# Kernel tuning notes

Hardware: AMD Instinct MI355X
Metric: run time of the kernel (lower is better)

## Reference

```python
import jax, jax.numpy as jnp
import numpy as np

D_MODEL, D_FF, H, DK, DV = 1024, 4096, 16, 64, 64
B, S = 16, 512
EPS = 1e-6

def layer_norm(x, g, b):
    mu = jnp.mean(x, axis=-1, keepdims=True)
    var = jnp.var(x, axis=-1, keepdims=True)
    return (x - mu) / jnp.sqrt(var + EPS) * g + b

def setup_inputs() -> dict:
    key = jax.random.key(0)
    ks = jax.random.split(key, 16)
    def lin(k, fan_in, fan_out):
        lim = 1.0 / np.sqrt(fan_in)
        kw, kb = jax.random.split(k)
        W = jax.random.uniform(kw, (fan_in, fan_out), jnp.float32, -lim, lim)
        b = jax.random.uniform(kb, (fan_out,), jnp.float32, -lim, lim)
        return W, b
    Wq, bq = lin(ks[0], D_MODEL, DK * H)
    Wk, bk = lin(ks[1], D_MODEL, DK * H)
    Wv, bv = lin(ks[2], D_MODEL, DV * H)
    Wo, bo = lin(ks[3], DV * H, D_MODEL)
    w1, b1 = lin(ks[4], D_MODEL, D_FF)   # conv1d k=1 == pointwise linear
    w2, b2 = lin(ks[5], D_FF, D_MODEL)
    return {
        "enc_inputs": jax.random.normal(ks[6], (B, S, D_MODEL), jnp.float32),
        "Wq": Wq, "bq": bq, "Wk": Wk, "bk": bk, "Wv": Wv, "bv": bv,
        "Wo": Wo, "bo": bo,
        "ln1_g": jnp.ones((D_MODEL,), jnp.float32), "ln1_b": jnp.zeros((D_MODEL,), jnp.float32),
        "w1": w1, "b1": b1, "w2": w2, "b2": b2,
        "ln2_g": jnp.ones((D_MODEL,), jnp.float32), "ln2_b": jnp.zeros((D_MODEL,), jnp.float32),
        "mask": jax.random.randint(ks[7], (B, S), 0, 2, jnp.int32),
        "max_neighbors": S,
    }

def reference(enc_inputs, Wq, bq, Wk, bk, Wv, bv, Wo, bo, ln1_g, ln1_b,
              w1, b1, w2, b2, ln2_g, ln2_b, mask, max_neighbors):
    x = enc_inputs  # [B, S, D]
    residual = x
    # projections -> [B, H, S, d]
    q = (x @ Wq + bq).reshape(B, S, H, DK).transpose(0, 2, 1, 3)
    k = (x @ Wk + bk).reshape(B, S, H, DK).transpose(0, 2, 1, 3)
    v = (x @ Wv + bv).reshape(B, S, H, DV).transpose(0, 2, 1, 3)
    scores = jnp.einsum('bhqd,bhkd->bhqk', q, k) / np.sqrt(DK)
    pad = (mask == 0)[:, None, None, :]  # [B,1,1,S] broadcasts over heads & query
    scores = jnp.where(pad, jnp.float32(-1e9), scores)
    attn = jax.nn.softmax(scores, axis=-1)
    ctx = jnp.einsum('bhqk,bhkd->bhqd', attn, v)
    ctx = ctx.transpose(0, 2, 1, 3).reshape(B, S, H * DV)
    ctx = ctx @ Wo + bo
    ctx = layer_norm(ctx + residual, ln1_g, ln1_b)
    # position-wise FFN (conv1d kernel=1 == linear)
    ff = jax.nn.relu(ctx @ w1 + b1) @ w2 + b2
    out = layer_norm(ff + ctx, ln2_g, ln2_b)
    return out, attn
```

## Files before the change

### kernel.cpp

```cpp
#include <hip/hip_runtime.h>
#include <hip/hip_bf16.h>

typedef unsigned short u16;
typedef __bf16 bf16x8 __attribute__((ext_vector_type(8)));
typedef float f32x4 __attribute__((ext_vector_type(4)));

static __device__ __forceinline__ float b2f(u16 x) {
    unsigned int u = ((unsigned int)x) << 16;
    float f; __builtin_memcpy(&f, &u, 4); return f;
}
static __device__ __forceinline__ float b2f_u32(unsigned int u) {
    float f; __builtin_memcpy(&f, &u, 4); return f;
}
static __device__ __forceinline__ u16 f2b(float f) {
    unsigned int u; __builtin_memcpy(&u, &f, 4);
    unsigned int lsb = (u >> 16) & 1u;
    u += 0x7fffu + lsb;
    return (u16)(u >> 16);
}

static __device__ __forceinline__ void gload16(const u16* g, u16* l) {
    __builtin_amdgcn_global_load_lds(
        (const __attribute__((address_space(1))) unsigned int*)g,
        (__attribute__((address_space(3))) unsigned int*)l, 16, 0, 0);
}

__global__ __launch_bounds__(256) void transpose_f2b(const float* __restrict__ src,
                                                     u16* __restrict__ dst,
                                                     int R, int C) {
    __shared__ u16 tile[32][33];
    int c0 = blockIdx.x * 32, r0 = blockIdx.y * 32;
    int tx = threadIdx.x & 31, ty = threadIdx.x >> 5;
    for (int i = ty; i < 32; i += 8) {
        int r = r0 + i, c = c0 + tx;
        tile[i][tx] = (r < R && c < C) ? f2b(src[(long)r * C + c]) : (u16)0;
    }
    __syncthreads();
    for (int i = ty; i < 32; i += 8) {
        int c = c0 + i, r = r0 + tx;
        if (c < C && r < R) dst[(long)c * R + r] = tile[tx][i];
    }
}

__global__ __launch_bounds__(256) void concat3(const float* a, const float* b, const float* c,
                                               float* out) {
    int i = blockIdx.x * 256 + threadIdx.x;
    if (i < 1024) out[i] = a[i];
    else if (i < 2048) out[i] = b[i - 1024];
    else if (i < 3072) out[i] = c[i - 2048];
}

__global__ __launch_bounds__(256) void conv_f2b(const float* __restrict__ src,
                                                u16* __restrict__ dst, long n) {
    long i = ((long)blockIdx.x * 256 + threadIdx.x) * 4;
    if (i >= n) return;
    float4 f = *(const float4*)(src + i);
    ushort4 o;
    o.x = f2b(f.x); o.y = f2b(f.y); o.z = f2b(f.z); o.w = f2b(f.w);
    *(ushort4*)(dst + i) = o;
}

__global__ __launch_bounds__(512, 1) void gemm_bt256(
    const u16* __restrict__ A, const u16* __restrict__ B,
    const float* __restrict__ bias, u16* __restrict__ C,
    int M, int N, int K, int lda, int ldb, int ldc, int relu, int nbx) {
    __shared__ __align__(16) u16 lds[2][4][8192];

    int nwg = gridDim.x;
    int id = blockIdx.x;
    int swz = (id & 7) * (nwg >> 3) + (id >> 3);
    int bx = swz % nbx, by = swz / nbx;
    long m0 = (long)by * 256, n0 = (long)bx * 256;

    int tid = threadIdx.x, lane = tid & 63, wave = tid >> 6;
    int lrow = lane & 15, quad = lane >> 4;
    int wm2 = wave >> 2;
    int wn2 = wave & 3;

    int laneRd = (lrow * 64 + quad * 16) ^ (((lrow >> 3) & 1) << 5);
    int Sl = (lane * 16) ^ (((lane >> 5) & 1) << 5);
    int wr = (Sl >> 6) & 15;
    int wb = Sl & 63;

    f32x4 acc[8][4];
#pragma unroll
    for (int i = 0; i < 8; i++)
#pragma unroll
        for (int j = 0; j < 4; j++) acc[i][j] = (f32x4){0.f, 0.f, 0.f, 0.f};
    bf16x8 af[4][2], bfr[2][2];

#define STAGE_HT(nb, ht, kt) do {                                              \
    const char* _gb = ((ht) < 2)                                               \
        ? (const char*)(A + (m0 + (ht) * 128) * lda)                           \
        : (const char*)(B + (n0 + ((ht) - 2) * 128) * ldb);                    \
    long _ld = (long)(((ht) < 2) ? lda : ldb) * 2;                             \
    _Pragma("unroll")                                                          \
    for (int j = 0; j < 2; j++) {                                              \
        int sub = j * 8 + wave;                                                \
        int srow = (sub >> 1) * 16 + wr;                                       \
        int scolb = (sub & 1) * 64 + wb;                                       \
        gload16((const u16*)(_gb + (long)srow * _ld + (long)(kt) * 128 + scolb),\
                &lds[nb][ht][sub << 9]);                                       \
    }                                                                          \
} while (0)

#define DSLOAD_A(qm) do {                                                      \
    const char* _p = _ab + ((qm) << 14);                                       \
    _Pragma("unroll") for (int mi = 0; mi < 4; mi++)                           \
    _Pragma("unroll") for (int kk = 0; kk < 2; kk++)                           \
        af[mi][kk] = *(const bf16x8*)(_p + ((mi * 4 + kk) << 10));             \
} while (0)

#define DSLOAD_B(qn) do {                                                      \
    const char* _p = _bb + ((qn) << 14);                                       \
    _Pragma("unroll") for (int ni = 0; ni < 2; ni++)                           \
    _Pragma("unroll") for (int kk = 0; kk < 2; kk++)                           \
        bfr[ni][kk] = *(const bf16x8*)(_p + ((ni * 8 + kk) << 10));            \
} while (0)

#define DOMFMA(qm, qn) do {                                                    \
    __builtin_amdgcn_s_setprio(1);                                             \
    _Pragma("unroll") for (int mi = 0; mi < 4; mi++)                           \
    _Pragma("unroll") for (int ni = 0; ni < 2; ni++)                           \
    _Pragma("unroll") for (int kk = 0; kk < 2; kk++)                           \
        acc[(qm) * 4 + mi][(qn) * 2 + ni] =                                    \
            __builtin_amdgcn_mfma_f32_16x16x32_bf16(                           \
                af[mi][kk], bfr[ni][kk], acc[(qm) * 4 + mi][(qn) * 2 + ni],    \
                0, 0, 0);                                                      \
    __builtin_amdgcn_s_setprio(0);                                             \
} while (0)

#define MIDBAR()  do { __builtin_amdgcn_s_barrier(); __builtin_amdgcn_sched_barrier(0); } while (0)
#define ENDBAR()  do { __builtin_amdgcn_sched_barrier(0); __builtin_amdgcn_s_barrier(); } while (0)

    int NT = K >> 6;
    STAGE_HT(0, 0, 0);
    STAGE_HT(0, 2, 0);
    STAGE_HT(0, 1, 0);
    STAGE_HT(0, 3, 0);

    for (int t = 0; t < NT - 1; t++) {
        int cur = t & 1, nxt = cur ^ 1;
        const char* _ab = (const char*)&lds[cur][0][0] + (wm2 << 11) + laneRd;
        const char* _bb = (const char*)&lds[cur][2][0] + (wn2 << 11) + laneRd;
        STAGE_HT(nxt, 0, t + 1);
        asm volatile("s_waitcnt vmcnt(6)" ::: "memory");
        MIDBAR();
        DSLOAD_A(0); DSLOAD_B(0); DOMFMA(0, 0);
        ENDBAR();
        STAGE_HT(nxt, 2, t + 1);
        asm volatile("s_waitcnt vmcnt(6)" ::: "memory");
        MIDBAR();
        DSLOAD_A(1); DOMFMA(1, 0);
        ENDBAR();
        STAGE_HT(nxt, 1, t + 1);
        asm volatile("s_waitcnt vmcnt(6)" ::: "memory");
        MIDBAR();
        DSLOAD_B(1); DOMFMA(1, 1);
        ENDBAR();
        STAGE_HT(nxt, 3, t + 1);
        MIDBAR();
        DSLOAD_A(0); DOMFMA(0, 1);
        ENDBAR();
    }
    {
        int cur = (NT - 1) & 1;
        const char* _ab = (const char*)&lds[cur][0][0] + (wm2 << 11) + laneRd;
        const char* _bb = (const char*)&lds[cur][2][0] + (wn2 << 11) + laneRd;
        asm volatile("s_waitcnt vmcnt(4)" ::: "memory");
        MIDBAR();
        DSLOAD_A(0); DSLOAD_B(0); DOMFMA(0, 0);
        ENDBAR();
        asm volatile("s_waitcnt vmcnt(2)" ::: "memory");
        MIDBAR();
        DSLOAD_A(1); DOMFMA(1, 0);
        ENDBAR();
        asm volatile("s_waitcnt vmcnt(0)" ::: "memory");
        MIDBAR();
        DSLOAD_B(1); DOMFMA(1, 1);
        ENDBAR();
        DSLOAD_A(0); DOMFMA(0, 1);
    }

#pragma unroll
    for (int mg = 0; mg < 8; mg++) {
        long row0 = m0 + (long)(((mg >> 2) * 8 + (mg & 3) * 2 + wm2) * 16 + quad * 4);
#pragma unroll
        for (int ng = 0; ng < 4; ng++) {
            long col = n0 + ((ng >> 1) * 8 + (ng & 1) * 4 + wn2) * 16 + lrow;
            float bv = bias ? bias[col] : 0.f;
#pragma unroll
            for (int r = 0; r < 4; r++) {
                float v = acc[mg][ng][r] + bv;
                if (relu) v = fmaxf(v, 0.f);
                C[(row0 + r) * ldc + col] = f2b(v);
            }
        }
    }
#undef STAGE_HT
#undef DSLOAD_A
#undef DSLOAD_B
#undef DOMFMA
}

__global__ __launch_bounds__(512, 1) void gemm_btn(
    const u16* __restrict__ A, const u16* __restrict__ B,
    const float* __restrict__ bias, u16* __restrict__ C,
    int K, int lda, int ldb, int ldc, int relu, int nbx) {
    __shared__ __align__(16) u16 lds[2][3][8192];

    int nwg = gridDim.x;
    int id = blockIdx.x;
    int swz = (id & 7) * (nwg >> 3) + (id >> 3);
    int bx = swz % nbx, by = swz / nbx;
    long m0 = (long)by * 128, n0 = (long)bx * 256;

    int tid = threadIdx.x, lane = tid & 63, wave = tid >> 6;
    int lrow = lane & 15, quad = lane >> 4;
    int wm2 = wave >> 2;
    int wn2 = wave & 3;

    int laneRd = (lrow * 64 + quad * 16) ^ (((lrow >> 3) & 1) << 5);
    int Sl = (lane * 16) ^ (((lane >> 5) & 1) << 5);
    int wr = (Sl >> 6) & 15;
    int wb = Sl & 63;

    f32x4 acc[4][4];
#pragma unroll
    for (int i = 0; i < 4; i++)
#pragma unroll
        for (int j = 0; j < 4; j++) acc[i][j] = (f32x4){0.f, 0.f, 0.f, 0.f};
    bf16x8 af[4][2], bfr[2][2];

#define STAGE_HT(nb, ht, kt) do {                                              \
    const char* _gb = ((ht) == 0)                                              \
        ? (const char*)(A + m0 * lda)                                          \
        : (const char*)(B + (n0 + ((ht) - 1) * 128) * ldb);                    \
    long _ld = (long)(((ht) == 0) ? lda : ldb) * 2;                            \
    _Pragma("unroll")                                                          \
    for (int j = 0; j < 2; j++) {                                              \
        int sub = j * 8 + wave;                                                \
        int srow = (sub >> 1) * 16 + wr;                                       \
        int scolb = (sub & 1) * 64 + wb;                                       \
        gload16((const u16*)(_gb + (long)srow * _ld + (long)(kt) * 128 + scolb),\
                &lds[nb][ht][sub << 9]);                                       \
    }                                                                          \
} while (0)

#define DSLOAD_A() do {                                                        \
    _Pragma("unroll") for (int mi = 0; mi < 4; mi++)                           \
    _Pragma("unroll") for (int kk = 0; kk < 2; kk++)                           \
        af[mi][kk] = *(const bf16x8*)(_ab + ((mi * 4 + kk) << 10));            \
} while (0)

#define DSLOAD_B(qn) do {                                                      \
    const char* _p = _b0 + (qn) * 16384;                                       \
    _Pragma("unroll") for (int ni = 0; ni < 2; ni++)                           \
    _Pragma("unroll") for (int kk = 0; kk < 2; kk++)                           \
        bfr[ni][kk] = *(const bf16x8*)(_p + ((ni * 8 + kk) << 10));            \
} while (0)

#define DOMFMA(qn) do {                                                        \
    __builtin_amdgcn_s_setprio(1);                                             \
    _Pragma("unroll") for (int mi = 0; mi < 4; mi++)                           \
    _Pragma("unroll") for (int ni = 0; ni < 2; ni++)                           \
    _Pragma("unroll") for (int kk = 0; kk < 2; kk++)                           \
        acc[mi][(qn) * 2 + ni] =                                               \
            __builtin_amdgcn_mfma_f32_16x16x32_bf16(                           \
                af[mi][kk], bfr[ni][kk], acc[mi][(qn) * 2 + ni], 0, 0, 0);     \
    __builtin_amdgcn_s_setprio(0);                                             \
} while (0)

    int NT = K >> 6;
    STAGE_HT(0, 0, 0);
    STAGE_HT(0, 1, 0);
    STAGE_HT(0, 2, 0);

    for (int t = 0; t < NT - 1; t++) {
        int cur = t & 1, nxt = cur ^ 1;
        const char* _ab = (const char*)&lds[cur][0][0] + (wm2 << 11) + laneRd;
        const char* _b0 = (const char*)&lds[cur][1][0] + (wn2 << 11) + laneRd;
        STAGE_HT(nxt, 0, t + 1);
        asm volatile("s_waitcnt vmcnt(4)" ::: "memory");
        MIDBAR();
        DSLOAD_A(); DSLOAD_B(0); DOMFMA(0);
        ENDBAR();
        STAGE_HT(nxt, 1, t + 1);
        STAGE_HT(nxt, 2, t + 1);
        asm volatile("s_waitcnt vmcnt(6)" ::: "memory");
        MIDBAR();
        DSLOAD_B(1); DOMFMA(1);
        ENDBAR();
    }
    {
        int cur = (NT - 1) & 1;
        const char* _ab = (const char*)&lds[cur][0][0] + (wm2 << 11) + laneRd;
        const char* _b0 = (const char*)&lds[cur][1][0] + (wn2 << 11) + laneRd;
        asm volatile("s_waitcnt vmcnt(2)" ::: "memory");
        MIDBAR();
        DSLOAD_A(); DSLOAD_B(0); DOMFMA(0);
        ENDBAR();
        asm volatile("s_waitcnt vmcnt(0)" ::: "memory");
        MIDBAR();
        DSLOAD_B(1); DOMFMA(1);
    }

#pragma unroll
    for (int mi = 0; mi < 4; mi++) {
        long row0 = m0 + (long)((mi * 2 + wm2) * 16 + quad * 4);
#pragma unroll
        for (int ng = 0; ng < 4; ng++) {
            long col = n0 + ((ng >> 1) * 8 + (ng & 1) * 4 + wn2) * 16 + lrow;
            float bv = bias ? bias[col] : 0.f;
#pragma unroll
            for (int r = 0; r < 4; r++) {
                float v = acc[mi][ng][r] + bv;
                if (relu) v = fmaxf(v, 0.f);
                C[(row0 + r) * ldc + col] = f2b(v);
            }
        }
    }
#undef STAGE_HT
#undef DSLOAD_A
#undef DSLOAD_B
#undef DOMFMA
#undef MIDBAR
#undef ENDBAR
}

__global__ __launch_bounds__(256) void split_v(const u16* __restrict__ qkv,
                                               u16* __restrict__ vT) {
    __shared__ u16 tile[32][33];
    int bh = blockIdx.z;
    int b = bh >> 4, h = bh & 15;
    int s0 = blockIdx.x * 32;
    int d0 = blockIdx.y * 32;
    int tx = threadIdx.x & 31, ty = threadIdx.x >> 5;
    for (int i = ty; i < 32; i += 8)
        tile[i][tx] = qkv[((long)(b * 512 + s0 + i)) * 3072 + 2048 + h * 64 + d0 + tx];
    __syncthreads();
    for (int i = ty; i < 32; i += 8)
        vT[((long)bh * 64 + d0 + i) * 512 + s0 + tx] = tile[tx][i];
}

__global__ __launch_bounds__(256) void attn_fused(
    const u16* __restrict__ qkv, const u16* __restrict__ vT,
    const int* __restrict__ mask, float* __restrict__ attnOut,
    u16* __restrict__ ctx) {
    __shared__ __align__(16) u16 s_k[2][64][72];
    __shared__ __align__(16) u16 s_p[4][16][68];
    __shared__ unsigned long long m_bits[8];

    int id = blockIdx.x;
    int t_ = id >> 3;
    int mtile = t_ & 7;
    int bh = (id & 7) + ((t_ >> 3) << 3);
    int b = bh >> 4, h = bh & 15;
    int tid = threadIdx.x, lane = tid & 63, wave = tid >> 6;
    int lrow = lane & 15, quad = lane >> 4;
    int m0 = mtile * 64;

    const u16* Qbase = qkv + (long)(b * 512) * 3072 + h * 64;
    const u16* Kbase = Qbase + 1024;
    const u16* vh = vT + (long)bh * 64 * 512;

    {
        int i0 = wave * 64 + lane;
        unsigned long long bl0 = __ballot(mask[b * 512 + i0] != 0);
        if (lane == 0) m_bits[wave] = bl0;
        unsigned long long bl1 = __ballot(mask[b * 512 + 256 + i0] != 0);
        if (lane == 0) m_bits[4 + wave] = bl1;
    }

    int sr = tid >> 3, sc = (tid & 7) * 8;
    int sr2 = (256 + tid) >> 3, sc2 = sc;
    *(uint4*)&s_k[0][sr][sc]  = *(const uint4*)(Qbase + (long)(m0 + sr) * 3072 + sc);
    *(uint4*)&s_k[0][sr2][sc2] = *(const uint4*)(Qbase + (long)(m0 + sr2) * 3072 + sc2);
    uint4 kreg[2];
    kreg[0] = *(const uint4*)(Kbase + (long)sr * 3072 + sc);
    kreg[1] = *(const uint4*)(Kbase + (long)sr2 * 3072 + sc2);
    __syncthreads();
    bf16x8 qf[2];
    qf[0] = *(const bf16x8*)&s_k[0][wave * 16 + lrow][0 + quad * 8];
    qf[1] = *(const bf16x8*)&s_k[0][wave * 16 + lrow][32 + quad * 8];
    __syncthreads();

    f32x4 sacc[32];
#pragma unroll
    for (int t = 0; t < 32; t++) sacc[t] = (f32x4){0.f, 0.f, 0.f, 0.f};

    for (int nc = 0; nc < 8; nc++) {
        int buf = nc & 1;
        *(uint4*)&s_k[buf][sr][sc]  = kreg[0];
        *(uint4*)&s_k[buf][sr2][sc2] = kreg[1];
        if (nc < 7) {
            kreg[0] = *(const uint4*)(Kbase + (long)((nc + 1) * 64 + sr) * 3072 + sc);
            kreg[1] = *(const uint4*)(Kbase + (long)((nc + 1) * 64 + sr2) * 3072 + sc2);
        }
        __syncthreads();
#pragma unroll
        for (int ni = 0; ni < 4; ni++) {
            bf16x8 b0 = *(const bf16x8*)&s_k[buf][ni * 16 + lrow][0 + quad * 8];
            bf16x8 b1 = *(const bf16x8*)&s_k[buf][ni * 16 + lrow][32 + quad * 8];
            int t = nc * 4 + ni;
            sacc[t] = __builtin_amdgcn_mfma_f32_16x16x32_bf16(qf[0], b0, sacc[t], 0, 0, 0);
            sacc[t] = __builtin_amdgcn_mfma_f32_16x16x32_bf16(qf[1], b1, sacc[t], 0, 0, 0);
        }
    }

    uint4 vreg[2];
    vreg[0] = *(const uint4*)(vh + (long)sr * 512 + sc);
    vreg[1] = *(const uint4*)(vh + (long)sr2 * 512 + sc2);

    float mx[4] = {-3.0e38f, -3.0e38f, -3.0e38f, -3.0e38f};
#pragma unroll
    for (int t = 0; t < 32; t++) {
        int col = t * 16 + lrow;
        int on = (int)((m_bits[col >> 6] >> (col & 63)) & 1ull);
#pragma unroll
        for (int r = 0; r < 4; r++) {
            float s = on ? sacc[t][r] * 0.125f : -1e9f;
            sacc[t][r] = s;
            mx[r] = fmaxf(mx[r], s);
        }
    }
#pragma unroll
    for (int off = 1; off < 16; off <<= 1)
#pragma unroll
        for (int r = 0; r < 4; r++) mx[r] = fmaxf(mx[r], __shfl_xor(mx[r], off));
    float sm[4] = {0.f, 0.f, 0.f, 0.f};
#pragma unroll
    for (int t = 0; t < 32; t++)
#pragma unroll
        for (int r = 0; r < 4; r++) {
            float e = __expf(sacc[t][r] - mx[r]);
            sacc[t][r] = e;
            sm[r] += e;
        }
#pragma unroll
    for (int off = 1; off < 16; off <<= 1)
#pragma unroll
        for (int r = 0; r < 4; r++) sm[r] += __shfl_xor(sm[r], off);
#pragma unroll
    for (int r = 0; r < 4; r++) sm[r] = 1.0f / sm[r];
#pragma unroll
    for (int t = 0; t < 32; t++)
#pragma unroll
        for (int r = 0; r < 4; r++) sacc[t][r] *= sm[r];

    f32x4 cacc[4];
#pragma unroll
    for (int ni = 0; ni < 4; ni++) cacc[ni] = (f32x4){0.f, 0.f, 0.f, 0.f};
    int prow = lane >> 4;
    int pseg = lane & 15;

    for (int nc = 0; nc < 8; nc++) {
        int buf = nc & 1;
        *(uint4*)&s_k[buf][sr][sc]  = vreg[0];
        *(uint4*)&s_k[buf][sr2][sc2] = vreg[1];
        if (nc < 7) {
            vreg[0] = *(const uint4*)(vh + (long)sr * 512 + (nc + 1) * 64 + sc);
            vreg[1] = *(const uint4*)(vh + (long)sr2 * 512 + (nc + 1) * 64 + sc2);
        }
#pragma unroll
        for (int t2 = 0; t2 < 4; t2++) {
            int t = nc * 4 + t2;
#pragma unroll
            for (int r = 0; r < 4; r++)
                s_p[wave][quad * 4 + r][t2 * 16 + lrow] = f2b(sacc[t][r]);
        }
        __syncthreads();

        {
            float* abase = attnOut + (long)bh * 512 * 512
                         + (long)(m0 + wave * 16) * 512 + nc * 64;
#pragma unroll
            for (int i = 0; i < 4; i++) {
                int row = i * 4 + prow;
                uint2 pv = *(const uint2*)&s_p[wave][row][pseg * 4];
                float4 o;
                o.x = b2f_u32(pv.x << 16);
                o.y = b2f_u32(pv.x & 0xffff0000u);
                o.z = b2f_u32(pv.y << 16);
                o.w = b2f_u32(pv.y & 0xffff0000u);
                *(float4*)(abase + (long)row * 512 + pseg * 4) = o;
            }
        }

#pragma unroll
        for (int kk = 0; kk < 2; kk++) {
            bf16x8 pf = *(const bf16x8*)&s_p[wave][lrow][kk * 32 + quad * 8];
#pragma unroll
            for (int ni = 0; ni < 4; ni++) {
                bf16x8 vf = *(const bf16x8*)&s_k[buf][ni * 16 + lrow][kk * 32 + quad * 8];
                cacc[ni] = __builtin_amdgcn_mfma_f32_16x16x32_bf16(pf, vf, cacc[ni], 0, 0, 0);
            }
        }
    }

    u16* crow = ctx + (long)(b * 512 + m0 + wave * 16 + quad * 4) * 1024 + h * 64 + lrow;
#pragma unroll
    for (int ni = 0; ni < 4; ni++)
#pragma unroll
        for (int r = 0; r < 4; r++) crow[(long)r * 1024 + ni * 16] = f2b(cacc[ni][r]);
}

__global__ __launch_bounds__(256) void add_ln(const u16* __restrict__ a,
                                              const void* __restrict__ r, int r_fp32,
                                              const float* __restrict__ g,
                                              const float* __restrict__ beta,
                                              void* __restrict__ out, int out_fp32) {
    long row = blockIdx.x;
    const u16* pa = a + row * 1024;
    int tid = threadIdx.x;
    float v[4];
    float sum = 0.f, sq = 0.f;
#pragma unroll
    for (int j = 0; j < 4; j++) {
        int c = tid + j * 256;
        float rv = r_fp32 ? ((const float*)r)[row * 1024 + c]
                          : b2f(((const u16*)r)[row * 1024 + c]);
        float x = b2f(pa[c]) + rv;
        v[j] = x;
        sum += x;
        sq += x * x;
    }
#pragma unroll
    for (int off = 32; off >= 1; off >>= 1) {
        sum += __shfl_xor(sum, off);
        sq += __shfl_xor(sq, off);
    }
    __shared__ float red[2][4];
    int wave = tid >> 6, lane = tid & 63;
    if (lane == 0) { red[0][wave] = sum; red[1][wave] = sq; }
    __syncthreads();
    sum = red[0][0] + red[0][1] + red[0][2] + red[0][3];
    sq = red[1][0] + red[1][1] + red[1][2] + red[1][3];
    float mu = sum * (1.f / 1024.f);
    float var = sq * (1.f / 1024.f) - mu * mu;
    float rstd = rsqrtf(var + 1e-6f);
#pragma unroll
    for (int j = 0; j < 4; j++) {
        int c = tid + j * 256;
        float y = (v[j] - mu) * rstd * g[c] + beta[c];
        if (out_fp32) ((float*)out)[row * 1024 + c] = y;
        else ((u16*)out)[row * 1024 + c] = f2b(y);
    }
}

extern "C" void kernel_launch(void* const* d_in, const int* in_sizes, int n_in,
                              void* d_out, int out_size, void* d_ws, size_t ws_size,
                              hipStream_t stream) {
    const float* x   = (const float*)d_in[0];
    const float* Wq  = (const float*)d_in[1];
    const float* bq  = (const float*)d_in[2];
    const float* Wk  = (const float*)d_in[3];
    const float* bk  = (const float*)d_in[4];
    const float* Wv  = (const float*)d_in[5];
    const float* bv  = (const float*)d_in[6];
    const float* Wo  = (const float*)d_in[7];
    const float* bo  = (const float*)d_in[8];
    const float* g1  = (const float*)d_in[9];
    const float* be1 = (const float*)d_in[10];
    const float* w1  = (const float*)d_in[11];
    const float* b1  = (const float*)d_in[12];
    const float* w2  = (const float*)d_in[13];
    const float* b2  = (const float*)d_in[14];
    const float* g2  = (const float*)d_in[15];
    const float* be2 = (const float*)d_in[16];
    const int* mask  = (const int*)d_in[17];

    float* out = (float*)d_out;
    float* attn = out + (long)8192 * 1024;

    char* w = (char*)d_ws;
    auto alloc = [&](size_t bytes) {
        char* p = w;
        w += (bytes + 255) & ~(size_t)255;
        return p;
    };
    u16* WqkvT = (u16*)alloc(3072L * 1024 * 2);
    u16* WoT   = (u16*)alloc(1024L * 1024 * 2);
    u16* w1T   = (u16*)alloc(4096L * 1024 * 2);
    u16* w2T   = (u16*)alloc(1024L * 4096 * 2);
    float* bqkv = (float*)alloc(3072L * 4);
    u16* xb    = (u16*)alloc(8192L * 1024 * 2);
    char* P1 = alloc(8192L * 4096 * 2);
    u16* qkv = (u16*)P1;
    u16* ff  = (u16*)P1;
    char* P2 = alloc(256L * 64 * 512 * 2);
    u16* vT = (u16*)P2;
    u16* y2 = (u16*)P2;
    u16* ctx = (u16*)alloc(8192L * 1024 * 2);
    u16* x1  = (u16*)alloc(8192L * 1024 * 2);
    u16* y   = (u16*)alloc(8192L * 1024 * 2);

    dim3 blk(256);

    transpose_f2b<<<dim3(32, 32), blk, 0, stream>>>(Wq, WqkvT, 1024, 1024);
    transpose_f2b<<<dim3(32, 32), blk, 0, stream>>>(Wk, WqkvT + 1024L * 1024, 1024, 1024);
    transpose_f2b<<<dim3(32, 32), blk, 0, stream>>>(Wv, WqkvT + 2048L * 1024, 1024, 1024);
    transpose_f2b<<<dim3(32, 32), blk, 0, stream>>>(Wo, WoT, 1024, 1024);
    transpose_f2b<<<dim3(128, 32), blk, 0, stream>>>(w1, w1T, 1024, 4096);
    transpose_f2b<<<dim3(32, 128), blk, 0, stream>>>(w2, w2T, 4096, 1024);
    concat3<<<12, blk, 0, stream>>>(bq, bk, bv, bqkv);
    conv_f2b<<<8192, blk, 0, stream>>>(x, xb, 8192L * 1024);

    gemm_bt256<<<dim3(384), dim3(512), 0, stream>>>(
        xb, WqkvT, bqkv, qkv, 8192, 3072, 1024, 1024, 1024, 3072, 0, 12);

    split_v<<<dim3(16, 2, 256), blk, 0, stream>>>(qkv, vT);

    attn_fused<<<dim3(2048), blk, 0, stream>>>(qkv, vT, mask, attn, ctx);

    gemm_btn<<<dim3(256), dim3(512), 0, stream>>>(
        ctx, WoT, bo, y, 1024, 1024, 1024, 1024, 0, 4);

    add_ln<<<8192, blk, 0, stream>>>(y, x, 1, g1, be1, x1, 0);

    gemm_bt256<<<dim3(512), dim3(512), 0, stream>>>(
        x1, w1T, b1, ff, 8192, 4096, 1024, 1024, 1024, 4096, 1, 16);

    gemm_btn<<<dim3(256), dim3(512), 0, stream>>>(
        ff, w2T, b2, y2, 4096, 4096, 4096, 1024, 0, 4);

    add_ln<<<8192, blk, 0, stream>>>(y2, x1, 0, g2, be2, out, 1);
}
```

Baseline: 812.8 us.

## Use split-K 256x256 tiles for FFN down-projection and fuse reduction into LayerNorm

The second FFN GEMM (8192x1024, K=4096) previously ran as 256 workgroups of 128x256 tiles. It now uses 256x256 tiles with a two-way K split, giving 128 output tiles times two halves, and each half writes fp32 partials to a new workspace buffer. The final LayerNorm kernel sums the two partials, adds the bias and residual, and normalizes. The larger tiles raise operand reuse per workgroup while keeping the workgroup count the same. In exchange it writes and reads two 32 MB fp32 partial buffers and needs extra workspace.

```diff
diff --git a/kernel.cpp b/kernel.cpp
--- a/kernel.cpp
+++ b/kernel.cpp
@@ -203,6 +203,148 @@
 #undef DOMFMA
 }
 
+__global__ __launch_bounds__(512, 1) void gemm_sk256(
+    const u16* __restrict__ A, const u16* __restrict__ B,
+    float* __restrict__ Cf,
+    int Ksplit, int lda, int ldb, int ldc, int nbx, long csize) {
+    __shared__ __align__(16) u16 lds[2][4][8192];
+
+    int id = blockIdx.x;
+    int sp = id & 1;
+    int id2 = id >> 1;
+    int nwg2 = gridDim.x >> 1;
+    int swz = (id2 & 7) * (nwg2 >> 3) + (id2 >> 3);
+    int bx = swz % nbx, by = swz / nbx;
+    long m0 = (long)by * 256, n0 = (long)bx * 256;
+
+    A += (long)sp * Ksplit;
+    B += (long)sp * Ksplit;
+    Cf += (long)sp * csize;
+
+    int tid = threadIdx.x, lane = tid & 63, wave = tid >> 6;
+    int lrow = lane & 15, quad = lane >> 4;
+    int wm2 = wave >> 2;
+    int wn2 = wave & 3;
+
+    int laneRd = (lrow * 64 + quad * 16) ^ (((lrow >> 3) & 1) << 5);
+    int Sl = (lane * 16) ^ (((lane >> 5) & 1) << 5);
+    int wr = (Sl >> 6) & 15;
+    int wb = Sl & 63;
+
+    f32x4 acc[8][4];
+#pragma unroll
+    for (int i = 0; i < 8; i++)
+#pragma unroll
+        for (int j = 0; j < 4; j++) acc[i][j] = (f32x4){0.f, 0.f, 0.f, 0.f};
+    bf16x8 af[4][2], bfr[2][2];
+
+#define STAGE_HT(nb, ht, kt) do {                                              \
+    const char* _gb = ((ht) < 2)                                               \
+        ? (const char*)(A + (m0 + (ht) * 128) * lda)                           \
+        : (const char*)(B + (n0 + ((ht) - 2) * 128) * ldb);                    \
+    long _ld = (long)(((ht) < 2) ? lda : ldb) * 2;                             \
+    _Pragma("unroll")                                                          \
+    for (int j = 0; j < 2; j++) {                                              \
+        int sub = j * 8 + wave;                                                \
+        int srow = (sub >> 1) * 16 + wr;                                       \
+        int scolb = (sub & 1) * 64 + wb;                                       \
+        gload16((const u16*)(_gb + (long)srow * _ld + (long)(kt) * 128 + scolb),\
+                &lds[nb][ht][sub << 9]);                                       \
+    }                                                                          \
+} while (0)
+
+#define DSLOAD_A(qm) do {                                                      \
+    const char* _p = _ab + ((qm) << 14);                                       \
+    _Pragma("unroll") for (int mi = 0; mi < 4; mi++)                           \
+    _Pragma("unroll") for (int kk = 0; kk < 2; kk++)                           \
+        af[mi][kk] = *(const bf16x8*)(_p + ((mi * 4 + kk) << 10));             \
+} while (0)
+
+#define DSLOAD_B(qn) do {                                                      \
+    const char* _p = _bb + ((qn) << 14);                                       \
+    _Pragma("unroll") for (int ni = 0; ni < 2; ni++)                           \
+    _Pragma("unroll") for (int kk = 0; kk < 2; kk++)                           \
+        bfr[ni][kk] = *(const bf16x8*)(_p + ((ni * 8 + kk) << 10));            \
+} while (0)
+
+#define DOMFMA(qm, qn) do {                                                    \
+    __builtin_amdgcn_s_setprio(1);                                             \
+    _Pragma("unroll") for (int mi = 0; mi < 4; mi++)                           \
+    _Pragma("unroll") for (int ni = 0; ni < 2; ni++)                           \
+    _Pragma("unroll") for (int kk = 0; kk < 2; kk++)                           \
+        acc[(qm) * 4 + mi][(qn) * 2 + ni] =                                    \
+            __builtin_amdgcn_mfma_f32_16x16x32_bf16(                           \
+                af[mi][kk], bfr[ni][kk], acc[(qm) * 4 + mi][(qn) * 2 + ni],    \
+                0, 0, 0);                                                      \
+    __builtin_amdgcn_s_setprio(0);                                             \
+} while (0)
+
+    int NT = Ksplit >> 6;
+    STAGE_HT(0, 0, 0);
+    STAGE_HT(0, 2, 0);
+    STAGE_HT(0, 1, 0);
+    STAGE_HT(0, 3, 0);
+
+    for (int t = 0; t < NT - 1; t++) {
+        int cur = t & 1, nxt = cur ^ 1;
+        const char* _ab = (const char*)&lds[cur][0][0] + (wm2 << 11) + laneRd;
+        const char* _bb = (const char*)&lds[cur][2][0] + (wn2 << 11) + laneRd;
+        STAGE_HT(nxt, 0, t + 1);
+        asm volatile("s_waitcnt vmcnt(6)" ::: "memory");
+        MIDBAR();
+        DSLOAD_A(0); DSLOAD_B(0); DOMFMA(0, 0);
+        ENDBAR();
+        STAGE_HT(nxt, 2, t + 1);
+        asm volatile("s_waitcnt vmcnt(6)" ::: "memory");
+        MIDBAR();
+        DSLOAD_A(1); DOMFMA(1, 0);
+        ENDBAR();
+        STAGE_HT(nxt, 1, t + 1);
+        asm volatile("s_waitcnt vmcnt(6)" ::: "memory");
+        MIDBAR();
+        DSLOAD_B(1); DOMFMA(1, 1);
+        ENDBAR();
+        STAGE_HT(nxt, 3, t + 1);
+        MIDBAR();
+        DSLOAD_A(0); DOMFMA(0, 1);
+        ENDBAR();
+    }
+    {
+        int cur = (NT - 1) & 1;
+        const char* _ab = (const char*)&lds[cur][0][0] + (wm2 << 11) + laneRd;
+        const char* _bb = (const char*)&lds[cur][2][0] + (wn2 << 11) + laneRd;
+        asm volatile("s_waitcnt vmcnt(4)" ::: "memory");
+        MIDBAR();
+        DSLOAD_A(0); DSLOAD_B(0); DOMFMA(0, 0);
+        ENDBAR();
+        asm volatile("s_waitcnt vmcnt(2)" ::: "memory");
+        MIDBAR();
+        DSLOAD_A(1); DOMFMA(1, 0);
+        ENDBAR();
+        asm volatile("s_waitcnt vmcnt(0)" ::: "memory");
+        MIDBAR();
+        DSLOAD_B(1); DOMFMA(1, 1);
+        ENDBAR();
+        DSLOAD_A(0); DOMFMA(0, 1);
+    }
+
+#pragma unroll
+    for (int mg = 0; mg < 8; mg++) {
+        long row0 = m0 + (long)(((mg >> 2) * 8 + (mg & 3) * 2 + wm2) * 16 + quad * 4);
+#pragma unroll
+        for (int ng = 0; ng < 4; ng++) {
+            long col = n0 + ((ng >> 1) * 8 + (ng & 1) * 4 + wn2) * 16 + lrow;
+#pragma unroll
+            for (int r = 0; r < 4; r++)
+                Cf[(row0 + r) * ldc + col] = acc[mg][ng][r];
+        }
+    }
+#undef STAGE_HT
+#undef DSLOAD_A
+#undef DSLOAD_B
+#undef DOMFMA
+}
+
 __global__ __launch_bounds__(512, 1) void gemm_btn(
     const u16* __restrict__ A, const u16* __restrict__ B,
     const float* __restrict__ bias, u16* __restrict__ C,
@@ -545,6 +687,47 @@
         float y = (v[j] - mu) * rstd * g[c] + beta[c];
         if (out_fp32) ((float*)out)[row * 1024 + c] = y;
         else ((u16*)out)[row * 1024 + c] = f2b(y);
+    }
+}
+
+__global__ __launch_bounds__(256) void add_ln2(const float* __restrict__ a1,
+                                               const float* __restrict__ a2,
+                                               const float* __restrict__ colb,
+                                               const u16* __restrict__ r,
+                                               const float* __restrict__ g,
+                                               const float* __restrict__ beta,
+                                               float* __restrict__ out) {
+    long row = blockIdx.x;
+    int tid = threadIdx.x;
+    float v[4];
+    float sum = 0.f, sq = 0.f;
+#pragma unroll
+    for (int j = 0; j < 4; j++) {
+        int c = tid + j * 256;
+        float x = a1[row * 1024 + c] + a2[row * 1024 + c] + colb[c]
+                + b2f(r[row * 1024 + c]);
+        v[j] = x;
+        sum += x;
+        sq += x * x;
+    }
+#pragma unroll
+    for (int off = 32; off >= 1; off >>= 1) {
+        sum += __shfl_xor(sum, off);
+        sq += __shfl_xor(sq, off);
+    }
+    __shared__ float red[2][4];
+    int wave = tid >> 6, lane = tid & 63;
+    if (lane == 0) { red[0][wave] = sum; red[1][wave] = sq; }
+    __syncthreads();
+    sum = red[0][0] + red[0][1] + red[0][2] + red[0][3];
+    sq = red[1][0] + red[1][1] + red[1][2] + red[1][3];
+    float mu = sum * (1.f / 1024.f);
+    float var = sq * (1.f / 1024.f) - mu * mu;
+    float rstd = rsqrtf(var + 1e-6f);
+#pragma unroll
+    for (int j = 0; j < 4; j++) {
+        int c = tid + j * 256;
+        out[row * 1024 + c] = (v[j] - mu) * rstd * g[c] + beta[c];
     }
 }
 
@@ -588,12 +771,11 @@
     char* P1 = alloc(8192L * 4096 * 2);
     u16* qkv = (u16*)P1;
     u16* ff  = (u16*)P1;
-    char* P2 = alloc(256L * 64 * 512 * 2);
-    u16* vT = (u16*)P2;
-    u16* y2 = (u16*)P2;
+    u16* vT  = (u16*)alloc(256L * 64 * 512 * 2);
     u16* ctx = (u16*)alloc(8192L * 1024 * 2);
     u16* x1  = (u16*)alloc(8192L * 1024 * 2);
     u16* y   = (u16*)alloc(8192L * 1024 * 2);
+    float* y2p = (float*)alloc(2L * 8192 * 1024 * 4);
 
     dim3 blk(256);
 
@@ -621,8 +803,8 @@
     gemm_bt256<<<dim3(512), dim3(512), 0, stream>>>(
         x1, w1T, b1, ff, 8192, 4096, 1024, 1024, 1024, 4096, 1, 16);
 
-    gemm_btn<<<dim3(256), dim3(512), 0, stream>>>(
-        ff, w2T, b2, y2, 4096, 4096, 4096, 1024, 0, 4);
-
-    add_ln<<<8192, blk, 0, stream>>>(y2, x1, 0, g2, be2, out, 1);
-}
+    gemm_sk256<<<dim3(256), dim3(512), 0, stream>>>(
+        ff, w2T, y2p, 2048, 4096, 4096, 1024, 4, 8192L * 1024);
+
+    add_ln2<<<8192, blk, 0, stream>>>(y2p, y2p + 8192L * 1024, b2, x1, g2, be2, out);
+}
```

After: 795.5 us. 1.02x faster.
